# Kernel tuning notes

Hardware: AMD Instinct MI355X
Metric: run time of the kernel (lower is better)

Reference implementation:

```python
import jax, jax.numpy as jnp
import numpy as np

B, S, D, H = 4, 2048, 1024, 16
DH = D // H


def setup_inputs() -> dict:
    key = jax.random.key(0)
    ks = jax.random.split(key, 5)
    std = 1.0 / np.sqrt(D)
    return {
        "x": jax.random.normal(ks[0], (B, S, D), dtype=jnp.float32),
        "mask": jnp.ones((S, S), dtype=bool),  # unused by the original forward
        "Wq": jax.random.normal(ks[1], (D, D), dtype=jnp.float32) * std,
        "Wk": jax.random.normal(ks[2], (D, D), dtype=jnp.float32) * std,
        "Wv": jax.random.normal(ks[3], (D, D), dtype=jnp.float32) * std,
        "Wout": jax.random.normal(ks[4], (D, D), dtype=jnp.float32) * std,
    }


def reference(x, mask, Wq, Wk, Wv, Wout):
    n, s, d = x.shape
    scale = 1.0 / np.sqrt(DH).astype(np.float32)
    q = (x @ Wq).reshape(n, s, H, DH)
    k = (x @ Wk).reshape(n, s, H, DH)
    v = (x @ Wv).reshape(n, s, H, DH)
    # scores [n, q, k, h]; softmax over k axis (dim=-2 in original)
    attn = jnp.einsum('nqhd,nkhd->nqkh', q, k) * scale
    attn = jax.nn.softmax(attn, axis=-2)
    z = jnp.einsum('nqkh,nkhd->nqhd', attn, v).reshape(n, s, d)
    z = jnp.einsum('nqd,de->nqe', z, Wout)
    return x + z
```

## Files before the change

### kernel.cpp

```cpp
#include <hip/hip_runtime.h>

#define Bn 4
#define Sn 2048
#define Dn 1024
#define Hn 16
#define DHn 64

typedef float f32x4 __attribute__((ext_vector_type(4)));
typedef short bf16x8 __attribute__((ext_vector_type(8)));
typedef unsigned short u16;
typedef unsigned int u32;
typedef unsigned short u16x8 __attribute__((ext_vector_type(8)));
typedef unsigned short u16x4 __attribute__((ext_vector_type(4)));
typedef u32 u32x4 __attribute__((ext_vector_type(4)));

union B8 { u32x4 u; bf16x8 s; u16x8 h; };

__device__ __forceinline__ u16 f2bf(float f){
  union { float f; u32 u; } v; v.f = f;
  return (u16)((v.u + 0x7fffu + ((v.u >> 16) & 1u)) >> 16);
}

__device__ __forceinline__ u32 pack_bf2(float lo, float hi){
  union { float f; u32 u; } a, b;
  a.f = lo; b.f = hi;
  return __builtin_amdgcn_perm(b.u, a.u, 0x07060302u);
}

#if __has_builtin(__builtin_amdgcn_exp2f)
#define EXP2(x) __builtin_amdgcn_exp2f(x)
#define QSCALE 0.18033688011112042f
#else
#define EXP2(x) __expf(x)
#define QSCALE 0.125f
#endif

#if __has_builtin(__builtin_amdgcn_global_load_lds)
#define G2L16(l, g) __builtin_amdgcn_global_load_lds((const __attribute__((address_space(1))) u32*)(g), \
                                                     (__attribute__((address_space(3))) u32*)(l), 16, 0, 0)
#else
#define G2L16(l, g) (*(bf16x8*)(l) = *(const bf16x8*)(g))
#endif

__global__ void prep_kernel(const float* __restrict__ x,
                            const float* __restrict__ Wq, const float* __restrict__ Wk,
                            const float* __restrict__ Wv, const float* __restrict__ Wo,
                            u16* __restrict__ xb, u16* __restrict__ wt_all){
  __shared__ u16 tile[64*66];
  const int t = threadIdx.x;
  if (blockIdx.x < 4096){
    size_t i = ((size_t)blockIdx.x * 256 + t) * 8;
    float4 f0 = *(const float4*)(x + i);
    float4 f1 = *(const float4*)(x + i + 4);
    u16x8 o;
    o[0]=f2bf(f0.x); o[1]=f2bf(f0.y); o[2]=f2bf(f0.z); o[3]=f2bf(f0.w);
    o[4]=f2bf(f1.x); o[5]=f2bf(f1.y); o[6]=f2bf(f1.z); o[7]=f2bf(f1.w);
    *(u16x8*)(xb + i) = o;
    return;
  }
  const int wi = blockIdx.x - 4096;
  const int z = wi >> 8, r8 = wi & 255;
  const int k0 = (r8 >> 4) * 64, n0 = (r8 & 15) * 64;
  const float* w = (z == 0) ? Wq : (z == 1) ? Wk : (z == 2) ? Wv : Wo;
  const float scale = (z == 0) ? QSCALE : 1.0f;
  u16* wt = wt_all + (size_t)z * Dn * Dn;
  #pragma unroll
  for (int i = 0; i < 4; i++){
    int idx = i*256 + t;
    int r = idx >> 4, c4 = (idx & 15) * 4;
    float4 f = *(const float4*)(w + (size_t)(k0 + r)*Dn + n0 + c4);
    tile[r*66 + c4 + 0] = f2bf(f.x * scale);
    tile[r*66 + c4 + 1] = f2bf(f.y * scale);
    tile[r*66 + c4 + 2] = f2bf(f.z * scale);
    tile[r*66 + c4 + 3] = f2bf(f.w * scale);
  }
  __syncthreads();
  #pragma unroll
  for (int i = 0; i < 4; i++){
    int idx = i*256 + t;
    int nr = idx >> 4, kc4 = (idx & 15) * 4;
    u16x4 o;
    o[0] = tile[(kc4+0)*66 + nr];
    o[1] = tile[(kc4+1)*66 + nr];
    o[2] = tile[(kc4+2)*66 + nr];
    o[3] = tile[(kc4+3)*66 + nr];
    *(u16x4*)(wt + (size_t)(n0 + nr)*Dn + k0 + kc4) = o;
  }
}

__launch_bounds__(256)
__global__ void gemm_qkv_kernel(const u16* __restrict__ xb, const u16* __restrict__ wt_all,
                                u16* __restrict__ qb, u16* __restrict__ kb, u16* __restrict__ vtb){
  __shared__ u16 As[128*32];
  __shared__ u16 Bs[128*32];
  __shared__ u16 Cs[128*136];
  const int t = threadIdx.x;
  const int wave = t >> 6, lane = t & 63;
  const int ln = lane & 15, quad = lane >> 4;
  const int wm = wave >> 1, wn = wave & 1;
  const int n0 = blockIdx.x * 128;
  const int m0 = blockIdx.y * 128;
  const int zsel = blockIdx.z;
  const u16* wt = wt_all + (size_t)zsel * Dn * Dn;

  f32x4 acc[4][4] = {};

  for (int kt = 0; kt < Dn; kt += 32){
    __syncthreads();
    #pragma unroll
    for (int i = 0; i < 2; i++){
      int idx = i*256 + t;
      int r = idx >> 2, c8 = (idx & 3) * 8;
      G2L16(&As[idx*8], xb + (size_t)(m0 + r)*Dn + kt + c8);
      G2L16(&Bs[idx*8], wt + (size_t)(n0 + r)*Dn + kt + c8);
    }
    __syncthreads();
    bf16x8 a[4], b[4];
    #pragma unroll
    for (int rb = 0; rb < 4; rb++) a[rb] = *(const bf16x8*)&As[(wm*64 + rb*16 + ln)*32 + quad*8];
    #pragma unroll
    for (int cb = 0; cb < 4; cb++) b[cb] = *(const bf16x8*)&Bs[(wn*64 + cb*16 + ln)*32 + quad*8];
    #pragma unroll
    for (int rb = 0; rb < 4; rb++)
      #pragma unroll
      for (int cb = 0; cb < 4; cb++)
        acc[rb][cb] = __builtin_amdgcn_mfma_f32_16x16x32_bf16(a[rb], b[cb], acc[rb][cb], 0, 0, 0);
  }

  if (zsel < 2){
    #pragma unroll
    for (int rb = 0; rb < 4; rb++)
      #pragma unroll
      for (int cb = 0; cb < 4; cb++)
        #pragma unroll
        for (int reg = 0; reg < 4; reg++)
          Cs[(wm*64 + rb*16 + quad*4 + reg)*136 + wn*64 + cb*16 + ln] = f2bf(acc[rb][cb][reg]);
  } else {
    #pragma unroll
    for (int rb = 0; rb < 4; rb++)
      #pragma unroll
      for (int cb = 0; cb < 4; cb++){
        u16x4 o;
        #pragma unroll
        for (int reg = 0; reg < 4; reg++) o[reg] = f2bf(acc[rb][cb][reg]);
        *(u16x4*)&Cs[(wn*64 + cb*16 + ln)*136 + wm*64 + rb*16 + quad*4] = o;
      }
  }
  __syncthreads();

  if (zsel < 2){
    u16* outp = (zsel == 0) ? qb : kb;
    #pragma unroll
    for (int i = 0; i < 8; i++){
      int idx = i*256 + t;
      int r = idx >> 4, c8 = (idx & 15) * 8;
      bf16x8 vdat = *(const bf16x8*)&Cs[r*136 + c8];
      int row = m0 + r, bb = row >> 11, s = row & 2047;
      int col = n0 + c8, hh = col >> 6, d = col & 63;
      *(bf16x8*)(outp + (((size_t)bb*Hn + hh)*Sn + s)*DHn + d) = vdat;
    }
  } else {
    #pragma unroll
    for (int i = 0; i < 8; i++){
      int idx = i*256 + t;
      int c = idx >> 4, r8 = (idx & 15) * 8;
      bf16x8 vdat = *(const bf16x8*)&Cs[c*136 + r8];
      int col = n0 + c, hh = col >> 6, d = col & 63;
      int row = m0 + r8, bb = row >> 11, s = row & 2047;
      *(bf16x8*)(vtb + (((size_t)bb*Hn + hh)*DHn + d)*Sn + s) = vdat;
    }
  }
}

__launch_bounds__(256, 2)
__global__ void attn_kernel(const u16* q, const u16* __restrict__ k,
                            const u16* __restrict__ vt, u16* z){
  __shared__ u16 Ks[2][64*72];
  __shared__ u16 Vs[2][64*72];
  const int t = threadIdx.x;
  const int wave = t >> 6, lane = t & 63;
  const int ln = lane & 15, quad = lane >> 4;
  const int qt = blockIdx.x, h = blockIdx.y, b = blockIdx.z;
  const size_t bh = (size_t)b * Hn + h;
  const int q0 = qt*256 + wave*64;
  const u16* qp = q + bh * Sn * DHn;
  const u16* kp = k + bh * Sn * DHn;
  const u16* vp = vt + bh * DHn * Sn;

  bf16x8 qf[4][2];
  #pragma unroll
  for (int n = 0; n < 4; n++)
    #pragma unroll
    for (int kq = 0; kq < 2; kq++)
      qf[n][kq] = *(const bf16x8*)(qp + (size_t)(q0 + n*16 + ln)*DHn + kq*32 + quad*8);

  f32x4 zacc[4][4] = {};
  float dacc[4] = {0.f, 0.f, 0.f, 0.f};

  bf16x8 rk[2], rv[2];

  #pragma unroll
  for (int i = 0; i < 2; i++){
    int idx = i*256 + t, r = idx >> 3, a = idx & 7;
    rk[i] = *(const bf16x8*)(kp + (size_t)r*DHn + a*8);
    rv[i] = *(const bf16x8*)(vp + (size_t)r*Sn + a*8);
  }
  #pragma unroll
  for (int i = 0; i < 2; i++){
    int idx = i*256 + t, r = idx >> 3, a = idx & 7;
    *(bf16x8*)&Ks[0][r*72 + a*8] = rk[i];
    int ksg = a >> 2, q1 = ((a&3)*2)&3, h1 = (a&3) >> 1;
    u16x4 lo = *(u16x4*)&rv[i];
    u16x4 hi = *((u16x4*)&rv[i] + 1);
    *(u16x4*)&Vs[0][r*72 + ksg*32 + q1*8 + h1*4] = lo;
    *(u16x4*)&Vs[0][r*72 + ksg*32 + ((q1+1)&3)*8 + h1*4] = hi;
  }

  for (int kt = 0; kt < Sn/64; kt++){
    const int cur = kt & 1;
    __syncthreads();

    if (kt + 1 < Sn/64){
      #pragma unroll
      for (int i = 0; i < 2; i++){
        int idx = i*256 + t, r = idx >> 3, a = idx & 7;
        rk[i] = *(const bf16x8*)(kp + (size_t)((kt+1)*64 + r)*DHn + a*8);
        rv[i] = *(const bf16x8*)(vp + (size_t)r*Sn + (kt+1)*64 + a*8);
      }
    }
    const u16* Kc = Ks[cur];
    const u16* Vc = Vs[cur];

    f32x4 sacc[4][4] = {};
    #pragma unroll
    for (int kq = 0; kq < 2; kq++){
      bf16x8 ka[4];
      #pragma unroll
      for (int mt = 0; mt < 4; mt++)
        ka[mt] = *(const bf16x8*)&Kc[(mt*16 + ln)*72 + kq*32 + quad*8];
      #pragma unroll
      for (int mt = 0; mt < 4; mt++)
        #pragma unroll
        for (int n = 0; n < 4; n++)
          sacc[mt][n] = __builtin_amdgcn_mfma_f32_16x16x32_bf16(ka[mt], qf[n][kq], sacc[mt][n], 0, 0, 0);
    }

    #pragma unroll
    for (int ks = 0; ks < 2; ks++){
      B8 pb[4];
      #pragma unroll
      for (int n = 0; n < 4; n++){
        f32x4 s0 = sacc[2*ks][n], s1 = sacc[2*ks+1][n];
        float a0 = EXP2(s0[0]), a1 = EXP2(s0[1]), a2 = EXP2(s0[2]), a3 = EXP2(s0[3]);
        float b0 = EXP2(s1[0]), b1 = EXP2(s1[1]), b2 = EXP2(s1[2]), b3 = EXP2(s1[3]);
        dacc[n] += ((a0 + a1) + (a2 + a3)) + ((b0 + b1) + (b2 + b3));
        pb[n].u = (u32x4){pack_bf2(a0, a1), pack_bf2(a2, a3), pack_bf2(b0, b1), pack_bf2(b2, b3)};
      }
      #pragma unroll
      for (int mtd = 0; mtd < 4; mtd++){
        bf16x8 va = *(const bf16x8*)&Vc[(mtd*16 + ln)*72 + ks*32 + quad*8];
        #pragma unroll
        for (int n = 0; n < 4; n++)
          zacc[mtd][n] = __builtin_amdgcn_mfma_f32_16x16x32_bf16(va, pb[n].s, zacc[mtd][n], 0, 0, 0);
      }
    }

    if (kt + 1 < Sn/64){
      const int nxt = (kt+1) & 1;
      #pragma unroll
      for (int i = 0; i < 2; i++){
        int idx = i*256 + t, r = idx >> 3, a = idx & 7;
        *(bf16x8*)&Ks[nxt][r*72 + a*8] = rk[i];
        int ksg = a >> 2, q1 = ((a&3)*2)&3, h1 = (a&3) >> 1;
        u16x4 lo = *(u16x4*)&rv[i];
        u16x4 hi = *((u16x4*)&rv[i] + 1);
        *(u16x4*)&Vs[nxt][r*72 + ksg*32 + q1*8 + h1*4] = lo;
        *(u16x4*)&Vs[nxt][r*72 + ksg*32 + ((q1+1)&3)*8 + h1*4] = hi;
      }
    }
  }

  float inv[4];
  #pragma unroll
  for (int n = 0; n < 4; n++){
    float d = dacc[n];
    d += __shfl_xor(d, 16, 64);
    d += __shfl_xor(d, 32, 64);
    inv[n] = 1.0f / d;
  }

  #pragma unroll
  for (int mtd = 0; mtd < 4; mtd++)
    #pragma unroll
    for (int n = 0; n < 4; n++){
      u16x4 o;
      #pragma unroll
      for (int j = 0; j < 4; j++) o[j] = f2bf(zacc[mtd][n][j] * inv[n]);
      *(u16x4*)(z + (bh*Sn + (size_t)(q0 + n*16 + ln))*DHn + mtd*16 + quad*4) = o;
    }
}

__launch_bounds__(256)
__global__ void gemm_out_kernel(const u16* __restrict__ zb, const u16* __restrict__ wt,
                                const float* __restrict__ x, float* __restrict__ out){
  __shared__ u16 As[128*32];
  __shared__ u16 Bs[128*32];
  const int t = threadIdx.x;
  const int wave = t >> 6, lane = t & 63;
  const int ln = lane & 15, quad = lane >> 4;
  const int wm = wave >> 1, wn = wave & 1;
  const int n0 = blockIdx.x * 128;
  const int m0 = blockIdx.y * 128;

  f32x4 acc[4][4] = {};

  for (int kt = 0; kt < Dn; kt += 32){
    int h = kt >> 6, d0 = kt & 63;
    __syncthreads();
    #pragma unroll
    for (int i = 0; i < 2; i++){
      int idx = i*256 + t;
      int r = idx >> 2, c8 = (idx & 3) * 8;
      int row = m0 + r;
      int bb = row >> 11, s = row & 2047;
      G2L16(&As[idx*8], zb + (((size_t)bb*Hn + h)*Sn + s)*DHn + d0 + c8);
      G2L16(&Bs[idx*8], wt + (size_t)(n0 + r)*Dn + kt + c8);
    }
    __syncthreads();
    bf16x8 a[4], b[4];
    #pragma unroll
    for (int rb = 0; rb < 4; rb++) a[rb] = *(const bf16x8*)&As[(wm*64 + rb*16 + ln)*32 + quad*8];
    #pragma unroll
    for (int cb = 0; cb < 4; cb++) b[cb] = *(const bf16x8*)&Bs[(wn*64 + cb*16 + ln)*32 + quad*8];
    #pragma unroll
    for (int rb = 0; rb < 4; rb++)
      #pragma unroll
      for (int cb = 0; cb < 4; cb++)
        acc[rb][cb] = __builtin_amdgcn_mfma_f32_16x16x32_bf16(a[rb], b[cb], acc[rb][cb], 0, 0, 0);
  }

  #pragma unroll
  for (int rb = 0; rb < 4; rb++)
    #pragma unroll
    for (int cb = 0; cb < 4; cb++)
      #pragma unroll
      for (int reg = 0; reg < 4; reg++){
        int row = m0 + wm*64 + rb*16 + quad*4 + reg;
        int col = n0 + wn*64 + cb*16 + ln;
        size_t off = (size_t)row*Dn + col;
        out[off] = acc[rb][cb][reg] + x[off];
      }
}

extern "C" void kernel_launch(void* const* d_in, const int* in_sizes, int n_in,
                              void* d_out, int out_size, void* d_ws, size_t ws_size,
                              hipStream_t stream){
  const float* x    = (const float*)d_in[0];
  const float* Wq   = (const float*)d_in[2];
  const float* Wk   = (const float*)d_in[3];
  const float* Wv   = (const float*)d_in[4];
  const float* Wout = (const float*)d_in[5];
  float* out = (float*)d_out;

  u16* ws = (u16*)d_ws;
  const size_t NW = (size_t)Dn * Dn;
  const size_t NX = (size_t)Bn * Sn * Dn;
  u16* wt  = ws;
  u16* xb  = wt + 4*NW;
  u16* qb  = xb + NX;
  u16* kb  = qb + NX;
  u16* vtb = kb + NX;

  dim3 blk(256);
  prep_kernel     <<<dim3(4096 + 1024), blk, 0, stream>>>(x, Wq, Wk, Wv, Wout, xb, wt);
  gemm_qkv_kernel <<<dim3(8,64,3), blk, 0, stream>>>(xb, wt, qb, kb, vtb);
  attn_kernel     <<<dim3(8,16,4), blk, 0, stream>>>(qb, kb, vtb, qb);
  gemm_out_kernel <<<dim3(8,64), blk, 0, stream>>>(qb, wt + 3*NW, x, out);
}
```

Before: 289.4 us.

## Double-buffer LDS tiles in both GEMMs and split attention QK by halves

The QKV and output GEMMs now use double-buffered LDS tiles. The next K-slice is loaded while MFMAs run on the current one, which cuts two barriers per step down to one. The QKV kernel reuses its staging buffer for the epilogue tile, so total LDS stays about the same. In the attention kernel, per-thread load and store offsets are computed once, and the score MFMAs are split into two half-tiles interleaved with exp and PV, which reduces live accumulator registers. The risk is that the single-barrier scheme depends on the asynchronous global-to-LDS loads finishing before the next barrier.

```diff
diff --git a/kernel.cpp b/kernel.cpp
--- a/kernel.cpp
+++ b/kernel.cpp
@@ -91,9 +91,7 @@
 __launch_bounds__(256)
 __global__ void gemm_qkv_kernel(const u16* __restrict__ xb, const u16* __restrict__ wt_all,
                                 u16* __restrict__ qb, u16* __restrict__ kb, u16* __restrict__ vtb){
-  __shared__ u16 As[128*32];
-  __shared__ u16 Bs[128*32];
-  __shared__ u16 Cs[128*136];
+  __shared__ u16 smem[128*136];
   const int t = threadIdx.x;
   const int wave = t >> 6, lane = t & 63;
   const int ln = lane & 15, quad = lane >> 4;
@@ -105,16 +103,30 @@
 
   f32x4 acc[4][4] = {};
 
-  for (int kt = 0; kt < Dn; kt += 32){
+  #pragma unroll
+  for (int i = 0; i < 2; i++){
+    int idx = i*256 + t;
+    int r = idx >> 2, c8 = (idx & 3) * 8;
+    G2L16(&smem[idx*8],        xb + (size_t)(m0 + r)*Dn + c8);
+    G2L16(&smem[4096 + idx*8], wt + (size_t)(n0 + r)*Dn + c8);
+  }
+
+  for (int ki = 0; ki < 32; ki++){
+    const int cur = ki & 1;
     __syncthreads();
-    #pragma unroll
-    for (int i = 0; i < 2; i++){
-      int idx = i*256 + t;
-      int r = idx >> 2, c8 = (idx & 3) * 8;
-      G2L16(&As[idx*8], xb + (size_t)(m0 + r)*Dn + kt + c8);
-      G2L16(&Bs[idx*8], wt + (size_t)(n0 + r)*Dn + kt + c8);
-    }
-    __syncthreads();
+    if (ki + 1 < 32){
+      const int nxt = 8192 * ((ki+1) & 1);
+      const int kt = (ki+1) * 32;
+      #pragma unroll
+      for (int i = 0; i < 2; i++){
+        int idx = i*256 + t;
+        int r = idx >> 2, c8 = (idx & 3) * 8;
+        G2L16(&smem[nxt + idx*8],        xb + (size_t)(m0 + r)*Dn + kt + c8);
+        G2L16(&smem[nxt + 4096 + idx*8], wt + (size_t)(n0 + r)*Dn + kt + c8);
+      }
+    }
+    const u16* As = &smem[8192*cur];
+    const u16* Bs = &smem[8192*cur + 4096];
     bf16x8 a[4], b[4];
     #pragma unroll
     for (int rb = 0; rb < 4; rb++) a[rb] = *(const bf16x8*)&As[(wm*64 + rb*16 + ln)*32 + quad*8];
@@ -127,6 +139,8 @@
         acc[rb][cb] = __builtin_amdgcn_mfma_f32_16x16x32_bf16(a[rb], b[cb], acc[rb][cb], 0, 0, 0);
   }
 
+  __syncthreads();
+  u16* Cs = smem;
   if (zsel < 2){
     #pragma unroll
     for (int rb = 0; rb < 4; rb++)
@@ -197,23 +211,29 @@
   f32x4 zacc[4][4] = {};
   float dacc[4] = {0.f, 0.f, 0.f, 0.f};
 
-  bf16x8 rk[2], rv[2];
-
+  int sr[2], sc[2], vc1[2], vc2[2];
   #pragma unroll
   for (int i = 0; i < 2; i++){
     int idx = i*256 + t, r = idx >> 3, a = idx & 7;
-    rk[i] = *(const bf16x8*)(kp + (size_t)r*DHn + a*8);
-    rv[i] = *(const bf16x8*)(vp + (size_t)r*Sn + a*8);
-  }
+    sr[i] = r; sc[i] = a*8;
+    int ksg = a >> 2, q1 = ((a&3)*2)&3, h1 = (a&3) >> 1;
+    vc1[i] = ksg*32 + q1*8 + h1*4;
+    vc2[i] = ksg*32 + (((q1+1)&3))*8 + h1*4;
+  }
+
+  bf16x8 rk[2], rv[2];
   #pragma unroll
   for (int i = 0; i < 2; i++){
-    int idx = i*256 + t, r = idx >> 3, a = idx & 7;
-    *(bf16x8*)&Ks[0][r*72 + a*8] = rk[i];
-    int ksg = a >> 2, q1 = ((a&3)*2)&3, h1 = (a&3) >> 1;
+    rk[i] = *(const bf16x8*)(kp + (size_t)sr[i]*DHn + sc[i]);
+    rv[i] = *(const bf16x8*)(vp + (size_t)sr[i]*Sn + sc[i]);
+  }
+  #pragma unroll
+  for (int i = 0; i < 2; i++){
+    *(bf16x8*)&Ks[0][sr[i]*72 + sc[i]] = rk[i];
     u16x4 lo = *(u16x4*)&rv[i];
     u16x4 hi = *((u16x4*)&rv[i] + 1);
-    *(u16x4*)&Vs[0][r*72 + ksg*32 + q1*8 + h1*4] = lo;
-    *(u16x4*)&Vs[0][r*72 + ksg*32 + ((q1+1)&3)*8 + h1*4] = hi;
+    *(u16x4*)&Vs[0][sr[i]*72 + vc1[i]] = lo;
+    *(u16x4*)&Vs[0][sr[i]*72 + vc2[i]] = hi;
   }
 
   for (int kt = 0; kt < Sn/64; kt++){
@@ -223,34 +243,32 @@
     if (kt + 1 < Sn/64){
       #pragma unroll
       for (int i = 0; i < 2; i++){
-        int idx = i*256 + t, r = idx >> 3, a = idx & 7;
-        rk[i] = *(const bf16x8*)(kp + (size_t)((kt+1)*64 + r)*DHn + a*8);
-        rv[i] = *(const bf16x8*)(vp + (size_t)r*Sn + (kt+1)*64 + a*8);
+        rk[i] = *(const bf16x8*)(kp + (size_t)((kt+1)*64 + sr[i])*DHn + sc[i]);
+        rv[i] = *(const bf16x8*)(vp + (size_t)sr[i]*Sn + (kt+1)*64 + sc[i]);
       }
     }
     const u16* Kc = Ks[cur];
     const u16* Vc = Vs[cur];
 
-    f32x4 sacc[4][4] = {};
-    #pragma unroll
-    for (int kq = 0; kq < 2; kq++){
-      bf16x8 ka[4];
-      #pragma unroll
-      for (int mt = 0; mt < 4; mt++)
-        ka[mt] = *(const bf16x8*)&Kc[(mt*16 + ln)*72 + kq*32 + quad*8];
-      #pragma unroll
-      for (int mt = 0; mt < 4; mt++)
+    #pragma unroll
+    for (int ks = 0; ks < 2; ks++){
+      f32x4 sacc[2][4] = {};
+      #pragma unroll
+      for (int kq = 0; kq < 2; kq++){
+        bf16x8 ka[2];
         #pragma unroll
-        for (int n = 0; n < 4; n++)
-          sacc[mt][n] = __builtin_amdgcn_mfma_f32_16x16x32_bf16(ka[mt], qf[n][kq], sacc[mt][n], 0, 0, 0);
-    }
-
-    #pragma unroll
-    for (int ks = 0; ks < 2; ks++){
+        for (int m2 = 0; m2 < 2; m2++)
+          ka[m2] = *(const bf16x8*)&Kc[((2*ks + m2)*16 + ln)*72 + kq*32 + quad*8];
+        #pragma unroll
+        for (int m2 = 0; m2 < 2; m2++)
+          #pragma unroll
+          for (int n = 0; n < 4; n++)
+            sacc[m2][n] = __builtin_amdgcn_mfma_f32_16x16x32_bf16(ka[m2], qf[n][kq], sacc[m2][n], 0, 0, 0);
+      }
       B8 pb[4];
       #pragma unroll
       for (int n = 0; n < 4; n++){
-        f32x4 s0 = sacc[2*ks][n], s1 = sacc[2*ks+1][n];
+        f32x4 s0 = sacc[0][n], s1 = sacc[1][n];
         float a0 = EXP2(s0[0]), a1 = EXP2(s0[1]), a2 = EXP2(s0[2]), a3 = EXP2(s0[3]);
         float b0 = EXP2(s1[0]), b1 = EXP2(s1[1]), b2 = EXP2(s1[2]), b3 = EXP2(s1[3]);
         dacc[n] += ((a0 + a1) + (a2 + a3)) + ((b0 + b1) + (b2 + b3));
@@ -269,13 +287,11 @@
       const int nxt = (kt+1) & 1;
       #pragma unroll
       for (int i = 0; i < 2; i++){
-        int idx = i*256 + t, r = idx >> 3, a = idx & 7;
-        *(bf16x8*)&Ks[nxt][r*72 + a*8] = rk[i];
-        int ksg = a >> 2, q1 = ((a&3)*2)&3, h1 = (a&3) >> 1;
+        *(bf16x8*)&Ks[nxt][sr[i]*72 + sc[i]] = rk[i];
         u16x4 lo = *(u16x4*)&rv[i];
         u16x4 hi = *((u16x4*)&rv[i] + 1);
-        *(u16x4*)&Vs[nxt][r*72 + ksg*32 + q1*8 + h1*4] = lo;
-        *(u16x4*)&Vs[nxt][r*72 + ksg*32 + ((q1+1)&3)*8 + h1*4] = hi;
+        *(u16x4*)&Vs[nxt][sr[i]*72 + vc1[i]] = lo;
+        *(u16x4*)&Vs[nxt][sr[i]*72 + vc2[i]] = hi;
       }
     }
   }
@@ -303,8 +319,7 @@
 __launch_bounds__(256)
 __global__ void gemm_out_kernel(const u16* __restrict__ zb, const u16* __restrict__ wt,
                                 const float* __restrict__ x, float* __restrict__ out){
-  __shared__ u16 As[128*32];
-  __shared__ u16 Bs[128*32];
+  __shared__ u16 smem[2][2][128*32];
   const int t = threadIdx.x;
   const int wave = t >> 6, lane = t & 63;
   const int ln = lane & 15, quad = lane >> 4;
@@ -314,19 +329,33 @@
 
   f32x4 acc[4][4] = {};
 
-  for (int kt = 0; kt < Dn; kt += 32){
-    int h = kt >> 6, d0 = kt & 63;
+  #pragma unroll
+  for (int i = 0; i < 2; i++){
+    int idx = i*256 + t;
+    int r = idx >> 2, c8 = (idx & 3) * 8;
+    int row = m0 + r, bb = row >> 11, s = row & 2047;
+    G2L16(&smem[0][0][idx*8], zb + (((size_t)bb*Hn + 0)*Sn + s)*DHn + 0 + c8);
+    G2L16(&smem[0][1][idx*8], wt + (size_t)(n0 + r)*Dn + c8);
+  }
+
+  for (int ki = 0; ki < 32; ki++){
+    const int cur = ki & 1;
     __syncthreads();
-    #pragma unroll
-    for (int i = 0; i < 2; i++){
-      int idx = i*256 + t;
-      int r = idx >> 2, c8 = (idx & 3) * 8;
-      int row = m0 + r;
-      int bb = row >> 11, s = row & 2047;
-      G2L16(&As[idx*8], zb + (((size_t)bb*Hn + h)*Sn + s)*DHn + d0 + c8);
-      G2L16(&Bs[idx*8], wt + (size_t)(n0 + r)*Dn + kt + c8);
-    }
-    __syncthreads();
+    if (ki + 1 < 32){
+      const int nxt = (ki+1) & 1;
+      const int kt = (ki+1) * 32;
+      const int hh = kt >> 6, d0 = kt & 63;
+      #pragma unroll
+      for (int i = 0; i < 2; i++){
+        int idx = i*256 + t;
+        int r = idx >> 2, c8 = (idx & 3) * 8;
+        int row = m0 + r, bb = row >> 11, s = row & 2047;
+        G2L16(&smem[nxt][0][idx*8], zb + (((size_t)bb*Hn + hh)*Sn + s)*DHn + d0 + c8);
+        G2L16(&smem[nxt][1][idx*8], wt + (size_t)(n0 + r)*Dn + kt + c8);
+      }
+    }
+    const u16* As = smem[cur][0];
+    const u16* Bs = smem[cur][1];
     bf16x8 a[4], b[4];
     #pragma unroll
     for (int rb = 0; rb < 4; rb++) a[rb] = *(const bf16x8*)&As[(wm*64 + rb*16 + ln)*32 + quad*8];
```

Result: no change. 283.8 us (-1.9%).
